# Optimization experiments

Measured on AMD Instinct MI355X. Metric: run time of the kernel, lower is better.

## Reference

```python
import jax, jax.numpy as jnp
import numpy as np

G, P, F, K = 256, 512, 4, 6   # graphs, nodes/graph, features, knn k
N = G * P

def _prelu(x, a):
    return jnp.where(x >= 0, x, a * x)

def _knn_edges(x):
    # per-graph brute-force kNN (k=6, no self loops), flow source->target
    xg = x.reshape(G, P, F)
    sq = jnp.sum(xg * xg, -1)                                   # [G,P]
    d = sq[:, :, None] + sq[:, None, :] - 2.0 * jnp.einsum('gpf,gqf->gpq', xg, xg)
    d = d + jnp.eye(P, dtype=x.dtype) * 1e10                    # exclude self
    _, idx = jax.lax.top_k(-d, K)                               # [G,P,K] neighbors
    off = (jnp.arange(G) * P)[:, None, None]
    src = (idx + off).reshape(-1)                               # message sources
    tgt = jnp.broadcast_to(jnp.arange(N).reshape(G, P, 1), (G, P, K)).reshape(-1)
    return src, tgt

def setup_inputs():
    key = jax.random.key(0)
    ks = jax.random.split(key, 8)
    f = lambda k, s: jax.random.normal(k, s, jnp.float32) * 0.1
    return {
        "x": jax.random.normal(ks[0], (N, F), jnp.float32),
        "batch": jnp.arange(N, dtype=jnp.int32) // P,
        "pre_W1": f(ks[1], (F, F)), "pre_b1": jnp.zeros((F,), jnp.float32),
        "pre_a1": jnp.full((F,), 0.25, jnp.float32),
        "pre_W2": f(ks[2], (F, F)), "pre_b2": jnp.zeros((F,), jnp.float32),
        "pre_a2": jnp.full((F,), 0.25, jnp.float32),
        "bn_g": jnp.ones((F,), jnp.float32), "bn_b": jnp.zeros((F,), jnp.float32),
        "act_a": jnp.full((F,), 0.25, jnp.float32),
        "conv_Wm": f(ks[3], (4, F, F)), "conv_bm": jnp.zeros((4, F), jnp.float32),
        "hlv_W1": f(ks[4], (5 * F, 5 * F)), "hlv_b1": jnp.zeros((5 * F,), jnp.float32),
        "hlv_W2": f(ks[5], (5 * F, 1)), "hlv_b2": jnp.zeros((1,), jnp.float32),
    }

def reference(x, batch, pre_W1, pre_b1, pre_a1, pre_W2, pre_b2, pre_a2,
              bn_g, bn_b, act_a, conv_Wm, conv_bm, hlv_W1, hlv_b1, hlv_W2, hlv_b2):
    src, tgt = _knn_edges(x)                                    # knn on raw x
    # pre_nn: Linear-PReLU-Linear-PReLU-BatchNorm (batch stats, training mode)
    h = _prelu(x @ pre_W1 + pre_b1, pre_a1)
    h = _prelu(h @ pre_W2 + pre_b2, pre_a2)
    mu = jnp.mean(h, 0)
    var = jnp.var(h, 0)
    h = (h - mu) / jnp.sqrt(var + 1e-5) * bn_g + bn_b
    xs = [h]
    for i in range(4):
        # GeneralConv (PyG defaults): sum-aggregate lin_msg(x_j) + identity skip
        msg = h[src] @ conv_Wm[i] + conv_bm[i]                  # [E,F]
        aggr = jax.ops.segment_sum(msg, tgt, num_segments=N)    # [N,F]
        h = _prelu(aggr + h, act_a)                             # shared PReLU act
        xs.append(h)
    hc = jnp.concatenate(xs, axis=-1)                           # JK 'cat' -> [N,5F]
    pooled = jax.ops.segment_sum(hc, batch, num_segments=G)     # global_add_pool
    out = jax.nn.relu(pooled @ hlv_W1 + hlv_b1) @ hlv_W2 + hlv_b2
    return out
```

## Files before the change

### kernel.cpp

```cpp
#include <hip/hip_runtime.h>

#define GG 256
#define PP 512
#define FF 4
#define KK 6
#define NN (GG*PP)

__device__ __forceinline__ unsigned umin_(unsigned a, unsigned b){ return a<b?a:b; }
__device__ __forceinline__ unsigned umax_(unsigned a, unsigned b){ return a>b?a:b; }
__device__ __forceinline__ float finf(){ return __int_as_float(0x7f800000); }

__device__ __forceinline__ unsigned mmap32(float d){
    int bb = __float_as_int(d);
    int t = bb >> 31;
    return (unsigned)(bb ^ (t | (int)0x80000000));
}

__device__ __forceinline__ void cas6_u64(uint64_t (&B)[6], uint64_t kv)
{
    bool c1 = kv < B[1]; bool c2 = kv < B[2]; bool c3 = kv < B[3];
    bool c4 = kv < B[4]; bool c5 = kv < B[5];
    B[0] = c1 ? B[1] : kv;
    B[1] = c2 ? B[2] : (c1 ? kv : B[1]);
    B[2] = c3 ? B[3] : (c2 ? kv : B[2]);
    B[3] = c4 ? B[4] : (c3 ? kv : B[3]);
    B[4] = c5 ? B[5] : (c4 ? kv : B[4]);
    B[5] = c5 ? kv : B[5];
}

#define INS7U(v){                                  \
    unsigned n0=umin_(M0,(v));                     \
    unsigned n1=umin_(M1,umax_((v),M0));           \
    unsigned n2=umin_(M2,umax_((v),M1));           \
    unsigned n3=umin_(M3,umax_((v),M2));           \
    unsigned n4=umin_(M4,umax_((v),M3));           \
    unsigned n5=umin_(M5,umax_((v),M4));           \
    unsigned n6=umin_(M6,umax_((v),M5));           \
    M0=n0;M1=n1;M2=n2;M3=n3;M4=n4;M5=n5;M6=n6; }

__global__ __launch_bounds__(512, 8) void scan_kernel(
    const float* __restrict__ x,
    const float* __restrict__ pre_W1, const float* __restrict__ pre_b1, const float* __restrict__ pre_a1,
    const float* __restrict__ pre_W2, const float* __restrict__ pre_b2, const float* __restrict__ pre_a2,
    float* __restrict__ bn_part,
    int* __restrict__ knn_idx)
{
    __shared__ float4   xm2s[PP];
    __shared__ float    sqs[PP];
    __shared__ unsigned ubuf[16*128];
    __shared__ float    Tv[128];
    __shared__ uint64_t pairbuf[128][6];
    __shared__ float    wred[8][8];

    ushort   (*gmp16)[128] = (ushort  (*)[128])ubuf;
    unsigned (*mbuf)[128]  = (unsigned(*)[128])ubuf;

    const int t = threadIdx.x;
    const int bid = blockIdx.x;
    const int g = bid >> 2, quarter = bid & 3;
    const int tbase = quarter * 128;
    const int gbase = g * PP;
    const int w = t >> 6, lane = t & 63;
    const int sid = w*2 + (lane >> 5);
    const int qb = sid * 32;
    const int tcol = t & 31;

    float4 xt = ((const float4*)x)[gbase + t];
    xm2s[t] = make_float4(-2.0f*xt.x, -2.0f*xt.y, -2.0f*xt.z, -2.0f*xt.w);
    sqs[t]  = xt.x*xt.x + xt.y*xt.y + xt.z*xt.z + xt.w*xt.w;
    if (quarter == 0){
        float h1[FF], h2[FF];
#pragma unroll
        for (int fo=0;fo<FF;fo++){
            float m = xt.x*pre_W1[0*FF+fo] + xt.y*pre_W1[1*FF+fo]
                    + xt.z*pre_W1[2*FF+fo] + xt.w*pre_W1[3*FF+fo] + pre_b1[fo];
            h1[fo] = m >= 0.0f ? m : pre_a1[fo]*m;
        }
#pragma unroll
        for (int fo=0;fo<FF;fo++){
            float m = h1[0]*pre_W2[0*FF+fo] + h1[1]*pre_W2[1*FF+fo]
                    + h1[2]*pre_W2[2*FF+fo] + h1[3]*pre_W2[3*FF+fo] + pre_b2[fo];
            h2[fo] = m >= 0.0f ? m : pre_a2[fo]*m;
        }
        float v[8];
#pragma unroll
        for (int f=0;f<4;f++){ v[f]=h2[f]; v[4+f]=h2[f]*h2[f]; }
#pragma unroll
        for (int off=32; off; off>>=1){
#pragma unroll
            for (int f=0;f<8;f++) v[f] += __shfl_down(v[f], off);
        }
        if (lane==0){
#pragma unroll
            for (int f=0;f<8;f++) wred[w][f]=v[f];
        }
    }
    __syncthreads();
    if (quarter == 0 && t < 8){
        float a=0;
#pragma unroll
        for (int w2=0;w2<8;w2++) a += wred[w2][t];
        bn_part[t*GG + g] = a;
    }

    float4 xp[4];
#pragma unroll
    for (int j=0;j<4;j++){
        float4 v = xm2s[tbase + tcol + 32*j];
        xp[j] = make_float4(-0.5f*v.x, -0.5f*v.y, -0.5f*v.z, -0.5f*v.w);
    }
    const float INF = finf();

#pragma unroll 1
    for (int grp=0; grp<2; grp++){
        float gm[4];
#pragma unroll
        for (int j=0;j<4;j++) gm[j]=INF;
#pragma unroll
        for (int i4=0;i4<4;i4++){
            const int q0 = qb + grp*16 + i4*4;
            float4 a0 = xm2s[q0],   a1 = xm2s[q0+1];
            float4 a2 = xm2s[q0+2], a3 = xm2s[q0+3];
            float4 sq = *(const float4*)&sqs[q0];
#pragma unroll
            for (int j=0;j<4;j++){
                float d0 = fmaf(a0.x,xp[j].x, fmaf(a0.y,xp[j].y, fmaf(a0.z,xp[j].z, fmaf(a0.w,xp[j].w, sq.x))));
                float d1 = fmaf(a1.x,xp[j].x, fmaf(a1.y,xp[j].y, fmaf(a1.z,xp[j].z, fmaf(a1.w,xp[j].w, sq.y))));
                float d2 = fmaf(a2.x,xp[j].x, fmaf(a2.y,xp[j].y, fmaf(a2.z,xp[j].z, fmaf(a2.w,xp[j].w, sq.z))));
                float d3 = fmaf(a3.x,xp[j].x, fmaf(a3.y,xp[j].y, fmaf(a3.z,xp[j].z, fmaf(a3.w,xp[j].w, sq.w))));
                gm[j] = fminf(gm[j], fminf(fminf(d0,d1), fminf(d2,d3)));
            }
        }
#pragma unroll
        for (int j=0;j<4;j++){
            unsigned u = mmap32(gm[j]);
            unsigned r = (u >> 16) + ((u & 0xFFFFu) ? 1u : 0u);
            r = umin_(r, 0xFFFFu);
            gmp16[sid*2 + grp][tcol + 32*j] = (ushort)r;
        }
    }
    __syncthreads();

    if (t < 128){
        unsigned M0=~0u,M1=~0u,M2=~0u,M3=~0u,M4=~0u,M5=~0u,M6=~0u;
#pragma unroll
        for (int r=0;r<32;r++){
            unsigned v = gmp16[r][t];
            INS7U(v);
        }
        unsigned Tc = M6 << 16;
        Tv[t] = (Tc & 0x80000000u) ? __uint_as_float(Tc ^ 0x80000000u)
                                   : __uint_as_float(~Tc);
    }
    __syncthreads();

    {
        float Tf[4];
#pragma unroll
        for (int j=0;j<4;j++) Tf[j] = Tv[tcol + 32*j];

        unsigned m[4];
#pragma unroll
        for (int j=0;j<4;j++) m[j]=0;
#pragma unroll 2
        for (int i4=0;i4<8;i4++){
            const int q0 = qb + i4*4;
            float4 a0 = xm2s[q0],   a1 = xm2s[q0+1];
            float4 a2 = xm2s[q0+2], a3 = xm2s[q0+3];
            float4 sq = *(const float4*)&sqs[q0];
#pragma unroll
            for (int j=0;j<4;j++){
                float d0 = fmaf(a0.x,xp[j].x, fmaf(a0.y,xp[j].y, fmaf(a0.z,xp[j].z, fmaf(a0.w,xp[j].w, sq.x))));
                float d1 = fmaf(a1.x,xp[j].x, fmaf(a1.y,xp[j].y, fmaf(a1.z,xp[j].z, fmaf(a1.w,xp[j].w, sq.y))));
                float d2 = fmaf(a2.x,xp[j].x, fmaf(a2.y,xp[j].y, fmaf(a2.z,xp[j].z, fmaf(a2.w,xp[j].w, sq.z))));
                float d3 = fmaf(a3.x,xp[j].x, fmaf(a3.y,xp[j].y, fmaf(a3.z,xp[j].z, fmaf(a3.w,xp[j].w, sq.w))));
                unsigned mm = m[j];
                mm = mm + mm + (d0 <= Tf[j] ? 1u : 0u);
                mm = mm + mm + (d1 <= Tf[j] ? 1u : 0u);
                mm = mm + mm + (d2 <= Tf[j] ? 1u : 0u);
                mm = mm + mm + (d3 <= Tf[j] ? 1u : 0u);
                m[j] = mm;
            }
        }
#pragma unroll
        for (int j=0;j<4;j++) mbuf[sid][tcol + 32*j] = m[j];
    }
    __syncthreads();

    uint64_t B[6];
#pragma unroll
    for (int j2=0;j2<6;j2++) B[j2] = ~0ull;
    if (t < 256){
        const int tgt = t >> 1, par = t & 1;
        const int pt = tbase + tgt;
        float4 xmq = xm2s[pt];
        float4 xq = make_float4(-0.5f*xmq.x, -0.5f*xmq.y, -0.5f*xmq.z, -0.5f*xmq.w);
#pragma unroll 1
        for (int r=par; r<16; r+=2){
            unsigned m = mbuf[r][tgt];
            const int base = r*32;
            while (m){
                int c = __builtin_clz(m);
                m &= ~(0x80000000u >> c);
                int idx = base + c;
                float4 a = xm2s[idx];
                float d = fmaf(a.x,xq.x, fmaf(a.y,xq.y, fmaf(a.z,xq.z, fmaf(a.w,xq.w, sqs[idx]))));
                uint64_t key = ((uint64_t)mmap32(d) << 32) | (unsigned)idx;
                key |= (uint64_t)0 - (uint64_t)(idx == pt);
                if (key < B[0]) cas6_u64(B, key);
            }
        }
        if (par == 1){
#pragma unroll
            for (int j2=0;j2<6;j2++) pairbuf[tgt][j2] = B[j2];
        }
    }
    __syncthreads();
    if (t < 256 && (t & 1) == 0){
        const int tgt = t >> 1;
#pragma unroll
        for (int j2=0;j2<6;j2++){
            uint64_t key = pairbuf[tgt][j2];
            if (key < B[0]) cas6_u64(B, key);
        }
#pragma unroll
        for (int j2=0;j2<6;j2++)
            knn_idx[j2*NN + gbase + tbase + tgt] = (int)(B[j2] & 0xFFFFFFFFull);
    }
}

__global__ __launch_bounds__(512) void graph_kernel(
    const float* __restrict__ x,
    const int* __restrict__ knn_idx,
    const float* __restrict__ bn_part,
    const float* __restrict__ pre_W1, const float* __restrict__ pre_b1, const float* __restrict__ pre_a1,
    const float* __restrict__ pre_W2, const float* __restrict__ pre_b2, const float* __restrict__ pre_a2,
    const float* __restrict__ bn_g, const float* __restrict__ bn_b,
    const float* __restrict__ act_a,
    const float* __restrict__ conv_Wm, const float* __restrict__ conv_bm,
    const float* __restrict__ hlv_W1, const float* __restrict__ hlv_b1,
    const float* __restrict__ hlv_W2, const float* __restrict__ hlv_b2,
    float* __restrict__ out)
{
    __shared__ float4 hbuf[PP];
    __shared__ float wred[8][4];
    __shared__ float pooled[20];
    __shared__ float stats[8];
    __shared__ float hid[20];
    const int g = blockIdx.x, p = threadIdx.x;
    const int gp = g*PP + p;

    if (p < 64){
        int vv = p>>3, j = p&7;
        float acc = 0.0f;
        for (int i=j;i<GG;i+=8) acc += bn_part[vv*GG + i];
        acc += __shfl_xor(acc,1); acc += __shfl_xor(acc,2); acc += __shfl_xor(acc,4);
        if (j==0) stats[vv] = acc;
    }
    __syncthreads();
    if (p < 4){
        float mu  = stats[p]   * (1.0f/NN);
        float var = stats[4+p] * (1.0f/NN) - mu*mu;
        stats[p]   = mu;
        stats[4+p] = 1.0f / sqrtf(var + 1e-5f);
    }

    float4 xt = ((const float4*)x)[gp];
    float h1[FF], h2[FF];
#pragma unroll
    for (int fo=0;fo<FF;fo++){
        float m = xt.x*pre_W1[0*FF+fo] + xt.y*pre_W1[1*FF+fo]
                + xt.z*pre_W1[2*FF+fo] + xt.w*pre_W1[3*FF+fo] + pre_b1[fo];
        h1[fo] = m >= 0.0f ? m : pre_a1[fo]*m;
    }
#pragma unroll
    for (int fo=0;fo<FF;fo++){
        float m = h1[0]*pre_W2[0*FF+fo] + h1[1]*pre_W2[1*FF+fo]
                + h1[2]*pre_W2[2*FF+fo] + h1[3]*pre_W2[3*FF+fo] + pre_b2[fo];
        h2[fo] = m >= 0.0f ? m : pre_a2[fo]*m;
    }
    __syncthreads();

    float hp[4];
#pragma unroll
    for (int f=0;f<4;f++)
        hp[f] = (h2[f] - stats[f]) * stats[4+f] * bn_g[f] + bn_b[f];
    hbuf[p] = make_float4(hp[0],hp[1],hp[2],hp[3]);
    int nb[KK];
#pragma unroll
    for (int j=0;j<KK;j++) nb[j] = knn_idx[j*NN + gp];

    auto block_accum = [&](const float* h, int slice){
        float v0=h[0], v1=h[1], v2=h[2], v3=h[3];
#pragma unroll
        for (int off=32; off; off>>=1){
            v0 += __shfl_down(v0,off); v1 += __shfl_down(v1,off);
            v2 += __shfl_down(v2,off); v3 += __shfl_down(v3,off);
        }
        int w = p>>6;
        if ((p&63)==0){ wred[w][0]=v0; wred[w][1]=v1; wred[w][2]=v2; wred[w][3]=v3; }
        __syncthreads();
        if (p < 4){
            float a=0;
#pragma unroll
            for (int w2=0;w2<8;w2++) a += wred[w2][p];
            pooled[slice*4+p] = a;
        }
        __syncthreads();
    };

    block_accum(hp, 0);

#pragma unroll 1
    for (int L=0; L<4; L++){
        float4 sm = make_float4(0.f,0.f,0.f,0.f);
#pragma unroll
        for (int j=0;j<KK;j++){
            float4 hn = hbuf[nb[j]];
            sm.x+=hn.x; sm.y+=hn.y; sm.z+=hn.z; sm.w+=hn.w;
        }
        const float* W  = conv_Wm + L*16;
        const float* bm = conv_bm + L*4;
        float nh[4];
#pragma unroll
        for (int fo=0;fo<4;fo++){
            float m = sm.x*W[0*4+fo] + sm.y*W[1*4+fo] + sm.z*W[2*4+fo] + sm.w*W[3*4+fo]
                    + 6.0f*bm[fo] + hp[fo];
            float a = act_a[fo];
            nh[fo] = m >= 0.0f ? m : a*m;
        }
        __syncthreads();
        hbuf[p] = make_float4(nh[0],nh[1],nh[2],nh[3]);
#pragma unroll
        for (int f=0;f<4;f++) hp[f]=nh[f];
        block_accum(hp, L+1);
    }

    if (p < 20){
        float acc = hlv_b1[p];
#pragma unroll 1
        for (int k2=0;k2<20;k2++) acc += pooled[k2]*hlv_W1[k2*20+p];
        hid[p] = acc > 0.0f ? acc : 0.0f;
    }
    __syncthreads();
    if (p == 0){
        float o = hlv_b2[0];
#pragma unroll 1
        for (int j=0;j<20;j++) o += hid[j]*hlv_W2[j];
        out[g] = o;
    }
}

extern "C" void kernel_launch(void* const* d_in, const int* in_sizes, int n_in,
                              void* d_out, int out_size, void* d_ws, size_t ws_size,
                              hipStream_t stream)
{
    const float* x      = (const float*)d_in[0];
    const float* pre_W1 = (const float*)d_in[2];
    const float* pre_b1 = (const float*)d_in[3];
    const float* pre_a1 = (const float*)d_in[4];
    const float* pre_W2 = (const float*)d_in[5];
    const float* pre_b2 = (const float*)d_in[6];
    const float* pre_a2 = (const float*)d_in[7];
    const float* bn_g   = (const float*)d_in[8];
    const float* bn_b   = (const float*)d_in[9];
    const float* act_a  = (const float*)d_in[10];
    const float* conv_Wm= (const float*)d_in[11];
    const float* conv_bm= (const float*)d_in[12];
    const float* hlv_W1 = (const float*)d_in[13];
    const float* hlv_b1 = (const float*)d_in[14];
    const float* hlv_W2 = (const float*)d_in[15];
    const float* hlv_b2 = (const float*)d_in[16];

    char* ws = (char*)d_ws;
    int*   knn     = (int*)ws;
    float* bn_part = (float*)(ws + (size_t)6*NN*sizeof(int));

    scan_kernel<<<GG*4, PP, 0, stream>>>(x, pre_W1,pre_b1,pre_a1,
                                         pre_W2,pre_b2,pre_a2, bn_part, knn);
    graph_kernel<<<GG, PP, 0, stream>>>(x, knn, bn_part,
                                        pre_W1,pre_b1,pre_a1, pre_W2,pre_b2,pre_a2,
                                        bn_g,bn_b, act_a, conv_Wm,conv_bm,
                                        hlv_W1,hlv_b1,hlv_W2,hlv_b2,
                                        (float*)d_out);
}
```

Measured before the change: 57.61 us.

## Fuse kNN scan and graph kernels into one cooperative launch with grid sync

Merges the kNN/batch-stat scan kernel and the per-graph message-passing kernel into one cooperative kernel separated by a grid-wide barrier. This removes the second launch and the gap between kernels, and keeps pre_nn outputs in registers so x is not reloaded. In exchange, all four quarter-blocks of each graph now redo the whole graph stage, with only quarter 0 writing the output, so that work is done four times. The fused path also depends on all 1024 blocks being co-resident, and falls back to the two-kernel path otherwise.

```diff
diff --git a/kernel.cpp b/kernel.cpp
--- a/kernel.cpp
+++ b/kernel.cpp
@@ -1,4 +1,5 @@
 #include <hip/hip_runtime.h>
+#include <hip/hip_cooperative_groups.h>
 
 #define GG 256
 #define PP 512
@@ -38,26 +39,20 @@
     unsigned n6=umin_(M6,umax_((v),M5));           \
     M0=n0;M1=n1;M2=n2;M3=n3;M4=n4;M5=n5;M6=n6; }
 
-__global__ __launch_bounds__(512, 8) void scan_kernel(
+template<bool FUSED>
+__device__ __forceinline__ void scan_body(
     const float* __restrict__ x,
     const float* __restrict__ pre_W1, const float* __restrict__ pre_b1, const float* __restrict__ pre_a1,
     const float* __restrict__ pre_W2, const float* __restrict__ pre_b2, const float* __restrict__ pre_a2,
-    float* __restrict__ bn_part,
-    int* __restrict__ knn_idx)
-{
-    __shared__ float4   xm2s[PP];
-    __shared__ float    sqs[PP];
-    __shared__ unsigned ubuf[16*128];
-    __shared__ float    Tv[128];
-    __shared__ uint64_t pairbuf[128][6];
-    __shared__ float    wred[8][8];
-
+    float* __restrict__ bn_part, int* __restrict__ knn_idx,
+    float4* xm2s, float* sqs, unsigned* ubuf, float* Tv,
+    uint64_t (*pairbuf)[6], float (*wred)[8],
+    int g, int quarter, float* h2out)
+{
     ushort   (*gmp16)[128] = (ushort  (*)[128])ubuf;
     unsigned (*mbuf)[128]  = (unsigned(*)[128])ubuf;
 
     const int t = threadIdx.x;
-    const int bid = blockIdx.x;
-    const int g = bid >> 2, quarter = bid & 3;
     const int tbase = quarter * 128;
     const int gbase = g * PP;
     const int w = t >> 6, lane = t & 63;
@@ -68,20 +63,22 @@
     float4 xt = ((const float4*)x)[gbase + t];
     xm2s[t] = make_float4(-2.0f*xt.x, -2.0f*xt.y, -2.0f*xt.z, -2.0f*xt.w);
     sqs[t]  = xt.x*xt.x + xt.y*xt.y + xt.z*xt.z + xt.w*xt.w;
+
+    float h1[FF], h2[FF];
+#pragma unroll
+    for (int fo=0;fo<FF;fo++){
+        float m = xt.x*pre_W1[0*FF+fo] + xt.y*pre_W1[1*FF+fo]
+                + xt.z*pre_W1[2*FF+fo] + xt.w*pre_W1[3*FF+fo] + pre_b1[fo];
+        h1[fo] = m >= 0.0f ? m : pre_a1[fo]*m;
+    }
+#pragma unroll
+    for (int fo=0;fo<FF;fo++){
+        float m = h1[0]*pre_W2[0*FF+fo] + h1[1]*pre_W2[1*FF+fo]
+                + h1[2]*pre_W2[2*FF+fo] + h1[3]*pre_W2[3*FF+fo] + pre_b2[fo];
+        h2[fo] = m >= 0.0f ? m : pre_a2[fo]*m;
+        h2out[fo] = h2[fo];
+    }
     if (quarter == 0){
-        float h1[FF], h2[FF];
-#pragma unroll
-        for (int fo=0;fo<FF;fo++){
-            float m = xt.x*pre_W1[0*FF+fo] + xt.y*pre_W1[1*FF+fo]
-                    + xt.z*pre_W1[2*FF+fo] + xt.w*pre_W1[3*FF+fo] + pre_b1[fo];
-            h1[fo] = m >= 0.0f ? m : pre_a1[fo]*m;
-        }
-#pragma unroll
-        for (int fo=0;fo<FF;fo++){
-            float m = h1[0]*pre_W2[0*FF+fo] + h1[1]*pre_W2[1*FF+fo]
-                    + h1[2]*pre_W2[2*FF+fo] + h1[3]*pre_W2[3*FF+fo] + pre_b2[fo];
-            h2[fo] = m >= 0.0f ? m : pre_a2[fo]*m;
-        }
         float v[8];
 #pragma unroll
         for (int f=0;f<4;f++){ v[f]=h2[f]; v[4+f]=h2[f]*h2[f]; }
@@ -229,6 +226,166 @@
     }
 }
 
+__device__ __forceinline__ void graph_body(
+    const float* __restrict__ h2in,
+    const int* __restrict__ knn_idx,
+    const float* __restrict__ bn_part,
+    const float* __restrict__ bn_g, const float* __restrict__ bn_b,
+    const float* __restrict__ act_a,
+    const float* __restrict__ conv_Wm, const float* __restrict__ conv_bm,
+    const float* __restrict__ hlv_W1, const float* __restrict__ hlv_b1,
+    const float* __restrict__ hlv_W2, const float* __restrict__ hlv_b2,
+    float4* hbuf, float (*wred)[8], float* stats, float* pooled, float* hid,
+    int g, bool writer, float* __restrict__ out)
+{
+    const int p = threadIdx.x;
+    const int gp = g*PP + p;
+    const int w = p>>6, lane = p&63;
+
+    if (p < 64){
+        int vv = p>>3, j = p&7;
+        float acc = 0.0f;
+        for (int i=j;i<GG;i+=8) acc += bn_part[vv*GG + i];
+        acc += __shfl_xor(acc,1); acc += __shfl_xor(acc,2); acc += __shfl_xor(acc,4);
+        if (j==0) stats[vv] = acc;
+    }
+    __syncthreads();
+    if (p < 4){
+        float mu  = stats[p]   * (1.0f/NN);
+        float var = stats[4+p] * (1.0f/NN) - mu*mu;
+        stats[p]   = mu;
+        stats[4+p] = 1.0f / sqrtf(var + 1e-5f);
+    }
+    __syncthreads();
+
+    float hp[4];
+#pragma unroll
+    for (int f=0;f<4;f++)
+        hp[f] = (h2in[f] - stats[f]) * stats[4+f] * bn_g[f] + bn_b[f];
+    hbuf[p] = make_float4(hp[0],hp[1],hp[2],hp[3]);
+    int nb[KK];
+#pragma unroll
+    for (int j=0;j<KK;j++) nb[j] = knn_idx[j*NN + gp];
+
+    auto block_accum = [&](const float* h, int slice){
+        float v0=h[0], v1=h[1], v2=h[2], v3=h[3];
+#pragma unroll
+        for (int off=32; off; off>>=1){
+            v0 += __shfl_down(v0,off); v1 += __shfl_down(v1,off);
+            v2 += __shfl_down(v2,off); v3 += __shfl_down(v3,off);
+        }
+        if (lane==0){ wred[w][0]=v0; wred[w][1]=v1; wred[w][2]=v2; wred[w][3]=v3; }
+        __syncthreads();
+        if (p < 4){
+            float a=0;
+#pragma unroll
+            for (int w2=0;w2<8;w2++) a += wred[w2][p];
+            pooled[slice*4+p] = a;
+        }
+        __syncthreads();
+    };
+
+    block_accum(hp, 0);
+
+#pragma unroll 1
+    for (int L=0; L<4; L++){
+        float4 sm = make_float4(0.f,0.f,0.f,0.f);
+#pragma unroll
+        for (int j=0;j<KK;j++){
+            float4 hn = hbuf[nb[j]];
+            sm.x+=hn.x; sm.y+=hn.y; sm.z+=hn.z; sm.w+=hn.w;
+        }
+        const float* W  = conv_Wm + L*16;
+        const float* bm = conv_bm + L*4;
+        float nh[4];
+#pragma unroll
+        for (int fo=0;fo<4;fo++){
+            float m = sm.x*W[0*4+fo] + sm.y*W[1*4+fo] + sm.z*W[2*4+fo] + sm.w*W[3*4+fo]
+                    + 6.0f*bm[fo] + hp[fo];
+            float a = act_a[fo];
+            nh[fo] = m >= 0.0f ? m : a*m;
+        }
+        __syncthreads();
+        hbuf[p] = make_float4(nh[0],nh[1],nh[2],nh[3]);
+#pragma unroll
+        for (int f=0;f<4;f++) hp[f]=nh[f];
+        block_accum(hp, L+1);
+    }
+
+    if (p < 20){
+        float acc = hlv_b1[p];
+#pragma unroll 1
+        for (int k2=0;k2<20;k2++) acc += pooled[k2]*hlv_W1[k2*20+p];
+        hid[p] = acc > 0.0f ? acc : 0.0f;
+    }
+    __syncthreads();
+    if (p == 0 && writer){
+        float o = hlv_b2[0];
+#pragma unroll 1
+        for (int j=0;j<20;j++) o += hid[j]*hlv_W2[j];
+        out[g] = o;
+    }
+}
+
+__global__ __launch_bounds__(512, 8) void fused_kernel(
+    const float* __restrict__ x,
+    const float* __restrict__ pre_W1, const float* __restrict__ pre_b1, const float* __restrict__ pre_a1,
+    const float* __restrict__ pre_W2, const float* __restrict__ pre_b2, const float* __restrict__ pre_a2,
+    const float* __restrict__ bn_g, const float* __restrict__ bn_b,
+    const float* __restrict__ act_a,
+    const float* __restrict__ conv_Wm, const float* __restrict__ conv_bm,
+    const float* __restrict__ hlv_W1, const float* __restrict__ hlv_b1,
+    const float* __restrict__ hlv_W2, const float* __restrict__ hlv_b2,
+    float* __restrict__ bn_part, int* __restrict__ knn_idx,
+    float* __restrict__ out)
+{
+    __shared__ float4   xm2s[PP];
+    __shared__ float    sqs[PP];
+    __shared__ unsigned ubuf[16*128];
+    __shared__ float    Tv[128];
+    __shared__ uint64_t pairbuf[128][6];
+    __shared__ float    wred[8][8];
+    __shared__ float    stats[8];
+    __shared__ float    pooled[20];
+    __shared__ float    hid[20];
+
+    const int bid = blockIdx.x;
+    const int g = bid >> 2, quarter = bid & 3;
+
+    float h2[4];
+    scan_body<true>(x, pre_W1,pre_b1,pre_a1, pre_W2,pre_b2,pre_a2,
+                    bn_part, knn_idx, xm2s, sqs, ubuf, Tv, pairbuf, wred,
+                    g, quarter, h2);
+
+    __threadfence();
+    cooperative_groups::this_grid().sync();
+
+    graph_body(h2, knn_idx, bn_part, bn_g,bn_b, act_a, conv_Wm,conv_bm,
+               hlv_W1,hlv_b1,hlv_W2,hlv_b2,
+               xm2s , wred, stats, pooled, hid,
+               g, quarter==0, out);
+}
+
+__global__ __launch_bounds__(512, 8) void scan_kernel(
+    const float* __restrict__ x,
+    const float* __restrict__ pre_W1, const float* __restrict__ pre_b1, const float* __restrict__ pre_a1,
+    const float* __restrict__ pre_W2, const float* __restrict__ pre_b2, const float* __restrict__ pre_a2,
+    float* __restrict__ bn_part, int* __restrict__ knn_idx)
+{
+    __shared__ float4   xm2s[PP];
+    __shared__ float    sqs[PP];
+    __shared__ unsigned ubuf[16*128];
+    __shared__ float    Tv[128];
+    __shared__ uint64_t pairbuf[128][6];
+    __shared__ float    wred[8][8];
+
+    const int bid = blockIdx.x;
+    float h2[4];
+    scan_body<false>(x, pre_W1,pre_b1,pre_a1, pre_W2,pre_b2,pre_a2,
+                     bn_part, knn_idx, xm2s, sqs, ubuf, Tv, pairbuf, wred,
+                     bid >> 2, bid & 3, h2);
+}
+
 __global__ __launch_bounds__(512) void graph_kernel(
     const float* __restrict__ x,
     const int* __restrict__ knn_idx,
@@ -243,29 +400,13 @@
     float* __restrict__ out)
 {
     __shared__ float4 hbuf[PP];
-    __shared__ float wred[8][4];
+    __shared__ float wred[8][8];
+    __shared__ float stats[8];
     __shared__ float pooled[20];
-    __shared__ float stats[8];
     __shared__ float hid[20];
     const int g = blockIdx.x, p = threadIdx.x;
-    const int gp = g*PP + p;
-
-    if (p < 64){
-        int vv = p>>3, j = p&7;
-        float acc = 0.0f;
-        for (int i=j;i<GG;i+=8) acc += bn_part[vv*GG + i];
-        acc += __shfl_xor(acc,1); acc += __shfl_xor(acc,2); acc += __shfl_xor(acc,4);
-        if (j==0) stats[vv] = acc;
-    }
-    __syncthreads();
-    if (p < 4){
-        float mu  = stats[p]   * (1.0f/NN);
-        float var = stats[4+p] * (1.0f/NN) - mu*mu;
-        stats[p]   = mu;
-        stats[4+p] = 1.0f / sqrtf(var + 1e-5f);
-    }
-
-    float4 xt = ((const float4*)x)[gp];
+
+    float4 xt = ((const float4*)x)[g*PP + p];
     float h1[FF], h2[FF];
 #pragma unroll
     for (int fo=0;fo<FF;fo++){
@@ -279,76 +420,9 @@
                 + h1[2]*pre_W2[2*FF+fo] + h1[3]*pre_W2[3*FF+fo] + pre_b2[fo];
         h2[fo] = m >= 0.0f ? m : pre_a2[fo]*m;
     }
-    __syncthreads();
-
-    float hp[4];
-#pragma unroll
-    for (int f=0;f<4;f++)
-        hp[f] = (h2[f] - stats[f]) * stats[4+f] * bn_g[f] + bn_b[f];
-    hbuf[p] = make_float4(hp[0],hp[1],hp[2],hp[3]);
-    int nb[KK];
-#pragma unroll
-    for (int j=0;j<KK;j++) nb[j] = knn_idx[j*NN + gp];
-
-    auto block_accum = [&](const float* h, int slice){
-        float v0=h[0], v1=h[1], v2=h[2], v3=h[3];
-#pragma unroll
-        for (int off=32; off; off>>=1){
-            v0 += __shfl_down(v0,off); v1 += __shfl_down(v1,off);
-            v2 += __shfl_down(v2,off); v3 += __shfl_down(v3,off);
-        }
-        int w = p>>6;
-        if ((p&63)==0){ wred[w][0]=v0; wred[w][1]=v1; wred[w][2]=v2; wred[w][3]=v3; }
-        __syncthreads();
-        if (p < 4){
-            float a=0;
-#pragma unroll
-            for (int w2=0;w2<8;w2++) a += wred[w2][p];
-            pooled[slice*4+p] = a;
-        }
-        __syncthreads();
-    };
-
-    block_accum(hp, 0);
-
-#pragma unroll 1
-    for (int L=0; L<4; L++){
-        float4 sm = make_float4(0.f,0.f,0.f,0.f);
-#pragma unroll
-        for (int j=0;j<KK;j++){
-            float4 hn = hbuf[nb[j]];
-            sm.x+=hn.x; sm.y+=hn.y; sm.z+=hn.z; sm.w+=hn.w;
-        }
-        const float* W  = conv_Wm + L*16;
-        const float* bm = conv_bm + L*4;
-        float nh[4];
-#pragma unroll
-        for (int fo=0;fo<4;fo++){
-            float m = sm.x*W[0*4+fo] + sm.y*W[1*4+fo] + sm.z*W[2*4+fo] + sm.w*W[3*4+fo]
-                    + 6.0f*bm[fo] + hp[fo];
-            float a = act_a[fo];
-            nh[fo] = m >= 0.0f ? m : a*m;
-        }
-        __syncthreads();
-        hbuf[p] = make_float4(nh[0],nh[1],nh[2],nh[3]);
-#pragma unroll
-        for (int f=0;f<4;f++) hp[f]=nh[f];
-        block_accum(hp, L+1);
-    }
-
-    if (p < 20){
-        float acc = hlv_b1[p];
-#pragma unroll 1
-        for (int k2=0;k2<20;k2++) acc += pooled[k2]*hlv_W1[k2*20+p];
-        hid[p] = acc > 0.0f ? acc : 0.0f;
-    }
-    __syncthreads();
-    if (p == 0){
-        float o = hlv_b2[0];
-#pragma unroll 1
-        for (int j=0;j<20;j++) o += hid[j]*hlv_W2[j];
-        out[g] = o;
-    }
+    graph_body(h2, knn_idx, bn_part, bn_g,bn_b, act_a, conv_Wm,conv_bm,
+               hlv_W1,hlv_b1,hlv_W2,hlv_b2,
+               hbuf, wred, stats, pooled, hid, g, true, out);
 }
 
 extern "C" void kernel_launch(void* const* d_in, const int* in_sizes, int n_in,
@@ -375,6 +449,23 @@
     char* ws = (char*)d_ws;
     int*   knn     = (int*)ws;
     float* bn_part = (float*)(ws + (size_t)6*NN*sizeof(int));
+    float* outp    = (float*)d_out;
+
+    int maxb = 0;
+    hipError_t qe = hipOccupancyMaxActiveBlocksPerMultiprocessor(&maxb, fused_kernel, PP, 0);
+    if (qe == hipSuccess && maxb >= 4){
+        void* args[] = {
+            (void*)&x, (void*)&pre_W1, (void*)&pre_b1, (void*)&pre_a1,
+            (void*)&pre_W2, (void*)&pre_b2, (void*)&pre_a2,
+            (void*)&bn_g, (void*)&bn_b, (void*)&act_a,
+            (void*)&conv_Wm, (void*)&conv_bm,
+            (void*)&hlv_W1, (void*)&hlv_b1, (void*)&hlv_W2, (void*)&hlv_b2,
+            (void*)&bn_part, (void*)&knn, (void*)&outp
+        };
+        hipError_t le = hipLaunchCooperativeKernel((const void*)fused_kernel,
+                                                   dim3(GG*4), dim3(PP), args, 0, stream);
+        if (le == hipSuccess) return;
+    }
 
     scan_kernel<<<GG*4, PP, 0, stream>>>(x, pre_W1,pre_b1,pre_a1,
                                          pre_W2,pre_b2,pre_a2, bn_part, knn);
@@ -382,5 +473,5 @@
                                         pre_W1,pre_b1,pre_a1, pre_W2,pre_b2,pre_a2,
                                         bn_g,bn_b, act_a, conv_Wm,conv_bm,
                                         hlv_W1,hlv_b1,hlv_W2,hlv_b2,
-                                        (float*)d_out);
-}
+                                        outp);
+}
```

Measured after the change: 57.69 us. No clear change (+0.1%).
